# Optimization experiments

Hardware: AMD Instinct MI355X
Metric: run time of the kernel (lower is better)

## Reference

```python
import jax, jax.numpy as jnp
import numpy as np

H = 2048       # hidden_size
I = 5504       # intermediate_size
E = 8          # num_experts
TOPK = 2       # num_experts_per_tok


def setup_inputs() -> dict:
    key = jax.random.key(0)
    ks = jax.random.split(key, 5)
    s = 0.02
    x = jax.random.normal(ks[0], (2, 2048, H), dtype=jnp.float32)
    router_w = jax.random.normal(ks[1], (E, H), dtype=jnp.float32) * s   # Linear weight [out,in]
    Wg = jax.random.normal(ks[2], (E, I, H), dtype=jnp.float32) * s      # gate_proj per expert
    Wu = jax.random.normal(ks[3], (E, I, H), dtype=jnp.float32) * s      # up_proj per expert
    Wd = jax.random.normal(ks[4], (E, H, I), dtype=jnp.float32) * s      # down_proj per expert
    return {"x": x, "router_w": router_w, "Wg": Wg, "Wu": Wu, "Wd": Wd}


def reference(x, router_w, Wg, Wu, Wd):
    B, S, Hh = x.shape
    xf = x.reshape(-1, Hh)                                  # [T, H]
    logits = xf @ router_w.T                                # [T, E]
    top_vals, top_idx = jax.lax.top_k(logits, TOPK)         # [T, K]
    top_w = jax.nn.softmax(top_vals, axis=-1)               # softmax over selected logits only
    # combine weight per (token, expert): zero if expert not selected
    combine = jnp.sum(jax.nn.one_hot(top_idx, E, dtype=xf.dtype) * top_w[..., None], axis=1)  # [T, E]

    out = jnp.zeros_like(xf)
    for e in range(E):  # fixed small expert loop (unrolled under jit)
        h = jax.nn.silu(xf @ Wg[e].T) * (xf @ Wu[e].T)      # [T, I]
        y = h @ Wd[e].T                                     # [T, H]
        out = out + combine[:, e:e + 1] * y
    return out.reshape(B, S, Hh)
```

## Files before the change

kernel.cpp:

```cpp
#include <hip/hip_runtime.h>
#include <cstdint>
#include <cstddef>

#define HDIM 2048
#define IDIM 5504
#define NEXP 8
#define NTOK 4096
#define NROWS (2 * NTOK)

#define NCT1 86
#define NRT1 16
#define NWG1 (NCT1 * NRT1 * NEXP)
#define NCT2 16
#define NRT2 16
#define NWG2 (NCT2 * NRT2 * NEXP)

typedef _Float16 half8 __attribute__((ext_vector_type(8)));
typedef _Float16 half4v __attribute__((ext_vector_type(4)));
typedef float floatx4 __attribute__((ext_vector_type(4)));

#define GLOAD16(g, l)                                                         \
  __builtin_amdgcn_global_load_lds(                                           \
      (const __attribute__((address_space(1))) void*)(g),                     \
      (__attribute__((address_space(3))) void*)(l), 16, 0, 0)

#define XH_OFF   0
#define HB_OFF   (XH_OFF + (size_t)NTOK * HDIM * 2)
#define BTOK_OFF (HB_OFF + (size_t)NROWS * IDIM * 2)
#define BW_OFF   (BTOK_OFF + 32768)
#define TOKP_OFF (BW_OFF + 32768)
#define TOKW_OFF (TOKP_OFF + 16384)
#define T2R_OFF  (TOKW_OFF + 32768)
#define META_OFF (T2R_OFF + 32768)
#define Y2_OFF   (META_OFF + 128)
#define WS_NEED_Y2 (Y2_OFF + (size_t)NROWS * HDIM * 2)
#define WG16_OFF (WS_NEED_Y2)
#define WU16_OFF (WG16_OFF + (size_t)NEXP * IDIM * HDIM * 2)
#define WD16_OFF (WU16_OFF + (size_t)NEXP * IDIM * HDIM * 2)
#define WS_NEED_W16 (WD16_OFF + (size_t)NEXP * HDIM * IDIM * 2)


__global__ void cvt_x_kernel(const float4* __restrict__ x, half4v* __restrict__ xh, int n4) {
  int i = blockIdx.x * blockDim.x + threadIdx.x;
  int st = gridDim.x * blockDim.x;
  for (; i < n4; i += st) {
    float4 v = x[i];
    half4v o = { (_Float16)v.x, (_Float16)v.y, (_Float16)v.z, (_Float16)v.w };
    xh[i] = o;
  }
}

__global__ void cvt_w_kernel(const float4* __restrict__ w, half8* __restrict__ o, int n8) {
  int i = blockIdx.x * blockDim.x + threadIdx.x;
  int st = gridDim.x * blockDim.x;
  for (; i < n8; i += st) {
    float4 a = w[2 * i], b = w[2 * i + 1];
    o[i] = half8{ (_Float16)a.x, (_Float16)a.y, (_Float16)a.z, (_Float16)a.w,
                  (_Float16)b.x, (_Float16)b.y, (_Float16)b.z, (_Float16)b.w };
  }
}

__global__ void router_kernel(const float* __restrict__ x, const float* __restrict__ rw,
                              int* __restrict__ tokp, float2* __restrict__ tokw,
                              int* __restrict__ cnt) {
  int t = blockIdx.x * 4 + (threadIdx.x >> 6);
  int lane = threadIdx.x & 63;
  const float4* xr = (const float4*)(x + (size_t)t * HDIM);
  float acc[NEXP];
#pragma unroll
  for (int e = 0; e < NEXP; ++e) acc[e] = 0.f;
#pragma unroll
  for (int it = 0; it < HDIM / 256; ++it) {
    float4 xv = xr[lane + 64 * it];
#pragma unroll
    for (int e = 0; e < NEXP; ++e) {
      float4 wv = ((const float4*)(rw + (size_t)e * HDIM))[lane + 64 * it];
      acc[e] += xv.x * wv.x + xv.y * wv.y + xv.z * wv.z + xv.w * wv.w;
    }
  }
#pragma unroll
  for (int off = 32; off > 0; off >>= 1) {
#pragma unroll
    for (int e = 0; e < NEXP; ++e) acc[e] += __shfl_xor(acc[e], off);
  }
  if (lane == 0) {
    int e0 = 0; float v0 = acc[0];
#pragma unroll
    for (int e = 1; e < NEXP; ++e) {
      if (acc[e] > v0) { v0 = acc[e]; e0 = e; }
    }
    int e1 = -1; float v1 = -3.0e38f;
#pragma unroll
    for (int e = 0; e < NEXP; ++e) {
      if (e == e0) continue;
      if (acc[e] > v1) { v1 = acc[e]; e1 = e; }
    }
    float w0 = 1.f / (1.f + __expf(v1 - v0));
    tokp[t] = e0 | (e1 << 8);
    tokw[t] = make_float2(w0, 1.f - w0);
    atomicAdd(&cnt[e0], 1);
    atomicAdd(&cnt[e1], 1);
  }
}

__global__ void scan_kernel(const int* __restrict__ cnt, int* __restrict__ offp) {
  if (threadIdx.x == 0) {
    int s = 0;
    for (int e = 0; e < NEXP; ++e) { offp[e] = s; s += cnt[e]; }
    offp[NEXP] = s;
  }
}

__global__ void scatter_kernel(const int* __restrict__ tokp, const float2* __restrict__ tokw,
                               const int* __restrict__ offp, int* __restrict__ cursor,
                               int* __restrict__ btok, float* __restrict__ bw,
                               int* __restrict__ t2r) {
  int t = blockIdx.x * blockDim.x + threadIdx.x;
  if (t >= NTOK) return;
  int p = tokp[t];
  float2 w = tokw[t];
  int e0 = p & 0xff, e1 = (p >> 8) & 0xff;
  int r0 = offp[e0] + atomicAdd(&cursor[e0], 1);
  btok[r0] = t; bw[r0] = w.x; t2r[2 * t] = r0;
  int r1 = offp[e1] + atomicAdd(&cursor[e1], 1);
  btok[r1] = t; bw[r1] = w.y; t2r[2 * t + 1] = r1;
}

__global__ void combine_kernel(const _Float16* __restrict__ y2, const int* __restrict__ t2r,
                               const float2* __restrict__ tokw, float* __restrict__ out) {
  int idx = blockIdx.x * 256 + threadIdx.x;
  int t = idx >> 9, c = (idx & 511) * 4;
  int r0 = t2r[2 * t], r1 = t2r[2 * t + 1];
  float2 w = tokw[t];
  half4v v0 = *(const half4v*)(y2 + (size_t)r0 * HDIM + c);
  half4v v1 = *(const half4v*)(y2 + (size_t)r1 * HDIM + c);
  float4 o;
  o.x = w.x * (float)v0[0] + w.y * (float)v1[0];
  o.y = w.x * (float)v0[1] + w.y * (float)v1[1];
  o.z = w.x * (float)v0[2] + w.y * (float)v1[2];
  o.w = w.x * (float)v0[3] + w.y * (float)v1[3];
  *(float4*)(out + (size_t)t * HDIM + c) = o;
}

__global__ __launch_bounds__(256, 4) void stage1_kernel(
    const _Float16* __restrict__ xh, const _Float16* __restrict__ Wg16,
    const int* __restrict__ offp, const int* __restrict__ btok, _Float16* __restrict__ hb) {
  int bid = blockIdx.x;
  int wg = (bid & 7) * (NWG1 / 8) + (bid >> 3);
  int rt = wg % NRT1;
  int ct = (wg / NRT1) % NCT1;
  int e  = wg / (NRT1 * NCT1);
  int base = offp[e];
  int ne = offp[e + 1] - base;
  if (rt * 128 >= ne) return;
  int valid = ne - rt * 128; if (valid > 128) valid = 128;
  int tid = threadIdx.x, lane = tid & 63, wave = tid >> 6;

  __shared__ __attribute__((aligned(16))) _Float16 As[2][128 * 32];
  __shared__ __attribute__((aligned(16))) _Float16 Bs[2][128 * 32];

  const char* abase = (const char*)xh;
  const char* bbase = (const char*)(Wg16 + (size_t)e * IDIM * HDIM);

  uint32_t aoffB[2], boffB[2];
#pragma unroll
  for (int i = 0; i < 2; ++i) {
    int L = wave * 128 + i * 64 + lane;
    int u = L >> 3, sc = (L & 7) ^ (u & 7);
    int r = 2 * u + (sc >> 2), q = sc & 3;
    int rr = (r < valid) ? r : (valid - 1);
    aoffB[i] = (uint32_t)(((uint32_t)btok[base + rt * 128 + rr] * HDIM + q * 8) * 2);
    size_t eloff = (r < 64) ? ((size_t)(ct * 64 + r) * HDIM)
                            : ((size_t)NEXP * IDIM * HDIM + (size_t)(ct * 64 + (r - 64)) * HDIM);
    boffB[i] = (uint32_t)((eloff + (size_t)q * 8) * 2);
  }
  int adst0 = __builtin_amdgcn_readfirstlane(wave * 2048);

  int wm = wave >> 1, wn = wave & 1;
  int lrow = lane & 15, kg = lane >> 4;

  int aoff[4], boff[4];
#pragma unroll
  for (int mi = 0; mi < 4; ++mi) {
    int r = wm * 64 + mi * 16 + lrow;
    int u = r >> 1, cc = (r & 1) * 4 + kg;
    aoff[mi] = u * 64 + ((cc ^ (u & 7)) * 8);
  }
#pragma unroll
  for (int f = 0; f < 4; ++f) {
    int rb = (f < 2) ? (wn * 32 + f * 16 + lrow) : (64 + wn * 32 + (f - 2) * 16 + lrow);
    int u = rb >> 1, cc = (rb & 1) * 4 + kg;
    boff[f] = u * 64 + ((cc ^ (u & 7)) * 8);
  }

  floatx4 acc[4][4] = {};

  auto stage = [&](int t, int buf) {
    uint32_t kb = (uint32_t)t * 64u;
#pragma unroll
    for (int i = 0; i < 2; ++i) {
      GLOAD16(abase + (aoffB[i] + kb), (char*)As[buf] + adst0 + i * 1024);
      GLOAD16(bbase + (boffB[i] + kb), (char*)Bs[buf] + adst0 + i * 1024);
    }
  };
  auto compute = [&](int buf) {
    half8 af[4], bf[4];
#pragma unroll
    for (int mi = 0; mi < 4; ++mi) af[mi] = *(const half8*)&As[buf][aoff[mi]];
#pragma unroll
    for (int f = 0; f < 4; ++f) bf[f] = *(const half8*)&Bs[buf][boff[f]];
#pragma unroll
    for (int mi = 0; mi < 4; ++mi)
#pragma unroll
      for (int f = 0; f < 4; ++f)
        acc[mi][f] = __builtin_amdgcn_mfma_f32_16x16x32_f16(af[mi], bf[f], acc[mi][f], 0, 0, 0);
  };

  int cur = 0;
  stage(0, 0);
  __syncthreads();
#pragma unroll 2
  for (int t = 0; t < HDIM / 32 - 1; ++t) {
    stage(t + 1, cur ^ 1);
    compute(cur);
    __syncthreads();
    cur ^= 1;
  }
  compute(cur);

  size_t hrow_base = (size_t)(base + rt * 128);
#pragma unroll
  for (int mi = 0; mi < 4; ++mi) {
#pragma unroll
    for (int j = 0; j < 4; ++j) {
      int r = wm * 64 + mi * 16 + kg * 4 + j;
      if (r < valid) {
#pragma unroll
        for (int f = 0; f < 2; ++f) {
          float g = acc[mi][f][j], u = acc[mi][f + 2][j];
          float hv = g / (1.f + __expf(-g)) * u;
          int c = ct * 64 + wn * 32 + f * 16 + lrow;
          hb[(hrow_base + r) * IDIM + c] = (_Float16)hv;
        }
      }
    }
  }
}

__global__ __launch_bounds__(256, 4) void stage2_kernel(
    const _Float16* __restrict__ hb, const _Float16* __restrict__ Wd16,
    const int* __restrict__ offp, _Float16* __restrict__ y2) {
  int bid = blockIdx.x;
  int wg = (bid & 7) * (NWG2 / 8) + (bid >> 3);
  int rt = wg % NRT2;
  int ct = (wg / NRT2) % NCT2;
  int e  = wg / (NRT2 * NCT2);
  int base = offp[e];
  int ne = offp[e + 1] - base;
  if (rt * 128 >= ne) return;
  int valid = ne - rt * 128; if (valid > 128) valid = 128;
  int tid = threadIdx.x, lane = tid & 63, wave = tid >> 6;

  __shared__ __attribute__((aligned(16))) _Float16 As[2][128 * 32];
  __shared__ __attribute__((aligned(16))) _Float16 Bs[2][128 * 32];

  const char* abase = (const char*)hb;
  const char* bbase = (const char*)(Wd16 + (size_t)e * HDIM * IDIM);

  uint32_t aoffB[2], boffB[2];
#pragma unroll
  for (int i = 0; i < 2; ++i) {
    int L = wave * 128 + i * 64 + lane;
    int u = L >> 3, sc = (L & 7) ^ (u & 7);
    int r = 2 * u + (sc >> 2), q = sc & 3;
    int rr = (r < valid) ? r : (valid - 1);
    aoffB[i] = (uint32_t)(((size_t)(base + rt * 128 + rr) * IDIM + (size_t)q * 8) * 2);
    boffB[i] = (uint32_t)(((size_t)(ct * 128 + r) * IDIM + (size_t)q * 8) * 2);
  }
  int adst0 = __builtin_amdgcn_readfirstlane(wave * 2048);

  int wm = wave >> 1, wn = wave & 1;
  int lrow = lane & 15, kg = lane >> 4;

  int aoff[4], boff[4];
#pragma unroll
  for (int mi = 0; mi < 4; ++mi) {
    int r = wm * 64 + mi * 16 + lrow;
    int u = r >> 1, cc = (r & 1) * 4 + kg;
    aoff[mi] = u * 64 + ((cc ^ (u & 7)) * 8);
  }
#pragma unroll
  for (int f = 0; f < 4; ++f) {
    int rb = wn * 64 + f * 16 + lrow;
    int u = rb >> 1, cc = (rb & 1) * 4 + kg;
    boff[f] = u * 64 + ((cc ^ (u & 7)) * 8);
  }

  floatx4 acc[4][4] = {};

  auto stage = [&](int t, int buf) {
    uint32_t kb = (uint32_t)t * 64u;
#pragma unroll
    for (int i = 0; i < 2; ++i) {
      GLOAD16(abase + (aoffB[i] + kb), (char*)As[buf] + adst0 + i * 1024);
      GLOAD16(bbase + (boffB[i] + kb), (char*)Bs[buf] + adst0 + i * 1024);
    }
  };
  auto compute = [&](int buf) {
    half8 af[4], bf[4];
#pragma unroll
    for (int mi = 0; mi < 4; ++mi) af[mi] = *(const half8*)&As[buf][aoff[mi]];
#pragma unroll
    for (int f = 0; f < 4; ++f) bf[f] = *(const half8*)&Bs[buf][boff[f]];
#pragma unroll
    for (int mi = 0; mi < 4; ++mi)
#pragma unroll
      for (int f = 0; f < 4; ++f)
        acc[mi][f] = __builtin_amdgcn_mfma_f32_16x16x32_f16(af[mi], bf[f], acc[mi][f], 0, 0, 0);
  };

  int cur = 0;
  stage(0, 0);
  __syncthreads();
#pragma unroll 2
  for (int t = 0; t < IDIM / 32 - 1; ++t) {
    stage(t + 1, cur ^ 1);
    compute(cur);
    __syncthreads();
    cur ^= 1;
  }
  compute(cur);

#pragma unroll
  for (int mi = 0; mi < 4; ++mi) {
#pragma unroll
    for (int j = 0; j < 4; ++j) {
      int r = wm * 64 + mi * 16 + kg * 4 + j;
      if (r < valid) {
        int grow = base + rt * 128 + r;
#pragma unroll
        for (int f = 0; f < 4; ++f) {
          int c = ct * 128 + wn * 64 + f * 16 + lrow;
          y2[(size_t)grow * HDIM + c] = (_Float16)acc[mi][f][j];
        }
      }
    }
  }
}

extern "C" void kernel_launch(void* const* d_in, const int* in_sizes, int n_in,
                              void* d_out, int out_size, void* d_ws, size_t ws_size,
                              hipStream_t stream) {
  const float* x  = (const float*)d_in[0];
  const float* rw = (const float*)d_in[1];
  const float* Wg = (const float*)d_in[2];
  const float* Wu = (const float*)d_in[3];
  const float* Wd = (const float*)d_in[4];
  float* out = (float*)d_out;

  char* ws = (char*)d_ws;
  _Float16* xh  = (_Float16*)(ws + XH_OFF);
  _Float16* hb  = (_Float16*)(ws + HB_OFF);
  int*      btok = (int*)(ws + BTOK_OFF);
  float*    bwv  = (float*)(ws + BW_OFF);
  int*      tokp = (int*)(ws + TOKP_OFF);
  float2*   tokw = (float2*)(ws + TOKW_OFF);
  int*      t2r  = (int*)(ws + T2R_OFF);
  int*      meta = (int*)(ws + META_OFF);
  _Float16* y2   = (_Float16*)(ws + Y2_OFF);
  _Float16* wg16 = (_Float16*)(ws + WG16_OFF);
  _Float16* wu16 = (_Float16*)(ws + WU16_OFF);
  _Float16* wd16 = (_Float16*)(ws + WD16_OFF);
  int* cnt = meta;
  int* offp = meta + 8;
  int* cursor = meta + 20;

  hipMemsetAsync(meta, 0, 128, stream);

  cvt_x_kernel<<<2048, 256, 0, stream>>>((const float4*)x, (half4v*)xh, NTOK * HDIM / 4);
  router_kernel<<<NTOK / 4, 256, 0, stream>>>(x, rw, tokp, tokw, cnt);
  scan_kernel<<<1, 64, 0, stream>>>(cnt, offp);
  scatter_kernel<<<NTOK / 256, 256, 0, stream>>>(tokp, tokw, offp, cursor, btok, bwv, t2r);

  int n8 = NEXP * IDIM * HDIM / 8;
  cvt_w_kernel<<<2048, 256, 0, stream>>>((const float4*)Wg, (half8*)wg16, n8);
  cvt_w_kernel<<<2048, 256, 0, stream>>>((const float4*)Wu, (half8*)wu16, n8);
  cvt_w_kernel<<<2048, 256, 0, stream>>>((const float4*)Wd, (half8*)wd16, n8);

  stage1_kernel<<<NWG1, 256, 0, stream>>>(xh, wg16, offp, btok, hb);
  stage2_kernel<<<NWG2, 256, 0, stream>>>(hb, wd16, offp, y2);
  combine_kernel<<<NTOK * HDIM / 4 / 256, 256, 0, stream>>>(y2, t2r, tokw, out);
}
```

Baseline: 1.297 ms.

## Rewrite expert GEMMs as 256x256 tiles with 8-wave ping-pong pipeline

Both grouped GEMM stages go from 128x128 tiles with 4 waves and a simple double buffer to 256x256 tiles (split into four 128x128 quadrants) with 8 waves and K=64 per step. The main loop now uses manual s_barrier and vmcnt waits, staged half-tile global-to-LDS loads into four slots, and raised MFMA priority, so loads overlap with compute. The aim is more operand reuse per byte loaded and fewer synchronisation stalls. The cost is 128KB of LDS per block, heavy register pressure, and a fragile hand-tuned barrier and wait schedule. Partially filled row tiles at expert boundaries also waste more compute.

```diff
diff --git a/kernel.cpp b/kernel.cpp
--- a/kernel.cpp
+++ b/kernel.cpp
@@ -8,12 +8,14 @@
 #define NTOK 4096
 #define NROWS (2 * NTOK)
 
-#define NCT1 86
-#define NRT1 16
-#define NWG1 (NCT1 * NRT1 * NEXP)
-#define NCT2 16
-#define NRT2 16
-#define NWG2 (NCT2 * NRT2 * NEXP)
+#define S1_NCT 43
+#define S1_NRT 8
+#define S1_NWG (S1_NCT * S1_NRT * NEXP)
+#define S1_NK  (HDIM / 64)
+#define S2_NCT 8
+#define S2_NRT 8
+#define S2_NWG (S2_NCT * S2_NRT * NEXP)
+#define S2_NK  (IDIM / 64)
 
 typedef _Float16 half8 __attribute__((ext_vector_type(8)));
 typedef _Float16 half4v __attribute__((ext_vector_type(4)));
@@ -23,6 +25,9 @@
   __builtin_amdgcn_global_load_lds(                                           \
       (const __attribute__((address_space(1))) void*)(g),                     \
       (__attribute__((address_space(3))) void*)(l), 16, 0, 0)
+
+#define SBAR()  asm volatile("s_barrier" ::: "memory")
+#define VMCNT(n) asm volatile("s_waitcnt vmcnt(" #n ")" ::: "memory")
 
 #define XH_OFF   0
 #define HB_OFF   (XH_OFF + (size_t)NTOK * HDIM * 2)
@@ -37,7 +42,6 @@
 #define WG16_OFF (WS_NEED_Y2)
 #define WU16_OFF (WG16_OFF + (size_t)NEXP * IDIM * HDIM * 2)
 #define WD16_OFF (WU16_OFF + (size_t)NEXP * IDIM * HDIM * 2)
-#define WS_NEED_W16 (WD16_OFF + (size_t)NEXP * HDIM * IDIM * 2)
 
 
 __global__ void cvt_x_kernel(const float4* __restrict__ x, half4v* __restrict__ xh, int n4) {
@@ -142,206 +146,321 @@
   *(float4*)(out + (size_t)t * HDIM + c) = o;
 }
 
-__global__ __launch_bounds__(256, 4) void stage1_kernel(
+#define MFMA_Q(Q, BF)                                                          \
+  {                                                                            \
+    __builtin_amdgcn_s_setprio(1);                                             \
+    _Pragma("unroll") for (int mi = 0; mi < 4; ++mi)                           \
+      _Pragma("unroll") for (int ni = 0; ni < 2; ++ni)                         \
+        _Pragma("unroll") for (int kk = 0; kk < 2; ++kk)                       \
+          acc[Q][mi][ni] = __builtin_amdgcn_mfma_f32_16x16x32_f16(             \
+              af[mi][kk], BF[ni][kk], acc[Q][mi][ni], 0, 0, 0);                \
+    __builtin_amdgcn_s_setprio(0);                                             \
+  }
+
+__global__ __launch_bounds__(512, 2) void stage1_kernel(
     const _Float16* __restrict__ xh, const _Float16* __restrict__ Wg16,
     const int* __restrict__ offp, const int* __restrict__ btok, _Float16* __restrict__ hb) {
   int bid = blockIdx.x;
-  int wg = (bid & 7) * (NWG1 / 8) + (bid >> 3);
-  int rt = wg % NRT1;
-  int ct = (wg / NRT1) % NCT1;
-  int e  = wg / (NRT1 * NCT1);
+  int wg = (bid & 7) * (S1_NWG / 8) + (bid >> 3);
+  int rt = wg % S1_NRT;
+  int ct = (wg / S1_NRT) % S1_NCT;
+  int e  = wg / (S1_NRT * S1_NCT);
   int base = offp[e];
   int ne = offp[e + 1] - base;
-  if (rt * 128 >= ne) return;
-  int valid = ne - rt * 128; if (valid > 128) valid = 128;
+  if (rt * 256 >= ne) return;
+  int valid = ne - rt * 256; if (valid > 256) valid = 256;
   int tid = threadIdx.x, lane = tid & 63, wave = tid >> 6;
-
-  __shared__ __attribute__((aligned(16))) _Float16 As[2][128 * 32];
-  __shared__ __attribute__((aligned(16))) _Float16 Bs[2][128 * 32];
+  int qr = wave >> 2, qc = wave & 3;
+  int lrow = lane & 15, kg = lane >> 4;
+
+  __shared__ __attribute__((aligned(16))) _Float16 Ah[4][128 * 64];
+  __shared__ __attribute__((aligned(16))) _Float16 Bh[4][128 * 64];
 
   const char* abase = (const char*)xh;
   const char* bbase = (const char*)(Wg16 + (size_t)e * IDIM * HDIM);
 
-  uint32_t aoffB[2], boffB[2];
-#pragma unroll
-  for (int i = 0; i < 2; ++i) {
-    int L = wave * 128 + i * 64 + lane;
-    int u = L >> 3, sc = (L & 7) ^ (u & 7);
-    int r = 2 * u + (sc >> 2), q = sc & 3;
-    int rr = (r < valid) ? r : (valid - 1);
-    aoffB[i] = (uint32_t)(((uint32_t)btok[base + rt * 128 + rr] * HDIM + q * 8) * 2);
-    size_t eloff = (r < 64) ? ((size_t)(ct * 64 + r) * HDIM)
-                            : ((size_t)NEXP * IDIM * HDIM + (size_t)(ct * 64 + (r - 64)) * HDIM);
-    boffB[i] = (uint32_t)((eloff + (size_t)q * 8) * 2);
-  }
-  int adst0 = __builtin_amdgcn_readfirstlane(wave * 2048);
-
-  int wm = wave >> 1, wn = wave & 1;
-  int lrow = lane & 15, kg = lane >> 4;
-
-  int aoff[4], boff[4];
+  uint32_t aoffB[2][2], boffB[2][2];
+#pragma unroll
+  for (int half = 0; half < 2; ++half) {
+#pragma unroll
+    for (int i = 0; i < 2; ++i) {
+      int L = i * 512 + tid;
+      int r = L >> 3, c = (L & 7) ^ (r & 7);
+      int rl = half * 128 + r;
+      int rr = (rl < valid) ? rl : (valid - 1);
+      aoffB[half][i] = (uint32_t)(((uint32_t)btok[base + rt * 256 + rr] * HDIM + c * 8) * 2);
+      size_t off = ((size_t)ct * 128 + r) * HDIM + (size_t)c * 8;
+      if (half) off += (size_t)NEXP * IDIM * HDIM;
+      boffB[half][i] = (uint32_t)(off * 2);
+    }
+  }
+  int dst0 = wave * 1024;
+  int dst1 = 8192 + wave * 1024;
+
+  int aro[4][2], bro[2][2];
 #pragma unroll
   for (int mi = 0; mi < 4; ++mi) {
-    int r = wm * 64 + mi * 16 + lrow;
-    int u = r >> 1, cc = (r & 1) * 4 + kg;
-    aoff[mi] = u * 64 + ((cc ^ (u & 7)) * 8);
-  }
-#pragma unroll
-  for (int f = 0; f < 4; ++f) {
-    int rb = (f < 2) ? (wn * 32 + f * 16 + lrow) : (64 + wn * 32 + (f - 2) * 16 + lrow);
-    int u = rb >> 1, cc = (rb & 1) * 4 + kg;
-    boff[f] = u * 64 + ((cc ^ (u & 7)) * 8);
-  }
-
-  floatx4 acc[4][4] = {};
-
-  auto stage = [&](int t, int buf) {
-    uint32_t kb = (uint32_t)t * 64u;
-#pragma unroll
-    for (int i = 0; i < 2; ++i) {
-      GLOAD16(abase + (aoffB[i] + kb), (char*)As[buf] + adst0 + i * 1024);
-      GLOAD16(bbase + (boffB[i] + kb), (char*)Bs[buf] + adst0 + i * 1024);
-    }
-  };
-  auto compute = [&](int buf) {
-    half8 af[4], bf[4];
-#pragma unroll
-    for (int mi = 0; mi < 4; ++mi) af[mi] = *(const half8*)&As[buf][aoff[mi]];
-#pragma unroll
-    for (int f = 0; f < 4; ++f) bf[f] = *(const half8*)&Bs[buf][boff[f]];
+    int r = qr * 64 + mi * 16 + lrow;
+#pragma unroll
+    for (int kk = 0; kk < 2; ++kk)
+      aro[mi][kk] = (r * 8 + ((kk * 4 + kg) ^ (r & 7))) * 8;
+  }
+#pragma unroll
+  for (int ni = 0; ni < 2; ++ni) {
+    int r = qc * 32 + ni * 16 + lrow;
+#pragma unroll
+    for (int kk = 0; kk < 2; ++kk)
+      bro[ni][kk] = (r * 8 + ((kk * 4 + kg) ^ (r & 7))) * 8;
+  }
+
+  floatx4 acc[4][4][2] = {};
+  half8 af[4][2], b0f[2][2], b1f[2][2];
+
+  auto STA = [&](int t, int half, _Float16* slot) {
+    uint32_t kb = (uint32_t)((t < S1_NK) ? t : (S1_NK - 1)) * 128u;
+    GLOAD16(abase + (aoffB[half][0] + kb), (char*)slot + dst0);
+    GLOAD16(abase + (aoffB[half][1] + kb), (char*)slot + dst1);
+  };
+  auto STB = [&](int t, int half, _Float16* slot) {
+    uint32_t kb = (uint32_t)((t < S1_NK) ? t : (S1_NK - 1)) * 128u;
+    GLOAD16(bbase + (boffB[half][0] + kb), (char*)slot + dst0);
+    GLOAD16(bbase + (boffB[half][1] + kb), (char*)slot + dst1);
+  };
+  auto LDA = [&](const _Float16* slot) {
 #pragma unroll
     for (int mi = 0; mi < 4; ++mi)
 #pragma unroll
-      for (int f = 0; f < 4; ++f)
-        acc[mi][f] = __builtin_amdgcn_mfma_f32_16x16x32_f16(af[mi], bf[f], acc[mi][f], 0, 0, 0);
-  };
-
-  int cur = 0;
-  stage(0, 0);
-  __syncthreads();
-#pragma unroll 2
-  for (int t = 0; t < HDIM / 32 - 1; ++t) {
-    stage(t + 1, cur ^ 1);
-    compute(cur);
-    __syncthreads();
-    cur ^= 1;
-  }
-  compute(cur);
-
-  size_t hrow_base = (size_t)(base + rt * 128);
-#pragma unroll
-  for (int mi = 0; mi < 4; ++mi) {
-#pragma unroll
-    for (int j = 0; j < 4; ++j) {
-      int r = wm * 64 + mi * 16 + kg * 4 + j;
-      if (r < valid) {
-#pragma unroll
-        for (int f = 0; f < 2; ++f) {
-          float g = acc[mi][f][j], u = acc[mi][f + 2][j];
-          float hv = g / (1.f + __expf(-g)) * u;
-          int c = ct * 64 + wn * 32 + f * 16 + lrow;
-          hb[(hrow_base + r) * IDIM + c] = (_Float16)hv;
+      for (int kk = 0; kk < 2; ++kk) af[mi][kk] = *(const half8*)&slot[aro[mi][kk]];
+  };
+  auto LDB0 = [&](const _Float16* slot) {
+#pragma unroll
+    for (int ni = 0; ni < 2; ++ni)
+#pragma unroll
+      for (int kk = 0; kk < 2; ++kk) b0f[ni][kk] = *(const half8*)&slot[bro[ni][kk]];
+  };
+  auto LDB1 = [&](const _Float16* slot) {
+#pragma unroll
+    for (int ni = 0; ni < 2; ++ni)
+#pragma unroll
+      for (int kk = 0; kk < 2; ++kk) b1f[ni][kk] = *(const half8*)&slot[bro[ni][kk]];
+  };
+
+  STB(0, 0, Bh[0]); STA(0, 0, Ah[0]); STA(0, 1, Ah[1]); STB(0, 1, Bh[1]);
+
+  for (int I = 0; I < S1_NK / 2; ++I) {
+    int t1 = 2 * I + 1, t2 = 2 * I + 2;
+    STB(t1, 0, Bh[2]);
+    VMCNT(2);
+    SBAR();
+    LDA(Ah[0]); LDB0(Bh[0]);
+    MFMA_Q(0, b0f);
+    SBAR();
+    STA(t1, 0, Ah[2]);
+    SBAR();
+    LDB1(Bh[1]);
+    MFMA_Q(1, b1f);
+    SBAR();
+    STA(t1, 1, Ah[3]); STB(t1, 1, Bh[3]);
+    SBAR();
+    LDA(Ah[1]);
+    MFMA_Q(2, b0f);
+    SBAR();
+    SBAR();
+    MFMA_Q(3, b1f);
+    SBAR();
+    STB(t2, 0, Bh[0]);
+    VMCNT(6);
+    SBAR();
+    LDA(Ah[2]); LDB0(Bh[2]);
+    MFMA_Q(0, b0f);
+    SBAR();
+    STA(t2, 0, Ah[0]);
+    VMCNT(4);
+    SBAR();
+    LDB1(Bh[3]);
+    MFMA_Q(1, b1f);
+    SBAR();
+    STA(t2, 1, Ah[1]); STB(t2, 1, Bh[1]);
+    SBAR();
+    LDA(Ah[3]);
+    MFMA_Q(2, b0f);
+    SBAR();
+    SBAR();
+    MFMA_Q(3, b1f);
+    SBAR();
+  }
+
+  size_t hrow_base = (size_t)(base + rt * 256);
+#pragma unroll
+  for (int qrow = 0; qrow < 2; ++qrow) {
+#pragma unroll
+    for (int mi = 0; mi < 4; ++mi) {
+#pragma unroll
+      for (int j = 0; j < 4; ++j) {
+        int r = qrow * 128 + qr * 64 + mi * 16 + kg * 4 + j;
+        if (r < valid) {
+#pragma unroll
+          for (int ni = 0; ni < 2; ++ni) {
+            float g = acc[qrow * 2][mi][ni][j];
+            float u = acc[qrow * 2 + 1][mi][ni][j];
+            float hv = g / (1.f + __expf(-g)) * u;
+            int cidx = ct * 128 + qc * 32 + ni * 16 + lrow;
+            hb[(hrow_base + r) * IDIM + cidx] = (_Float16)hv;
+          }
         }
       }
     }
   }
 }
 
-__global__ __launch_bounds__(256, 4) void stage2_kernel(
+__global__ __launch_bounds__(512, 2) void stage2_kernel(
     const _Float16* __restrict__ hb, const _Float16* __restrict__ Wd16,
     const int* __restrict__ offp, _Float16* __restrict__ y2) {
   int bid = blockIdx.x;
-  int wg = (bid & 7) * (NWG2 / 8) + (bid >> 3);
-  int rt = wg % NRT2;
-  int ct = (wg / NRT2) % NCT2;
-  int e  = wg / (NRT2 * NCT2);
+  int wg = (bid & 7) * (S2_NWG / 8) + (bid >> 3);
+  int rt = wg % S2_NRT;
+  int ct = (wg / S2_NRT) % S2_NCT;
+  int e  = wg / (S2_NRT * S2_NCT);
   int base = offp[e];
   int ne = offp[e + 1] - base;
-  if (rt * 128 >= ne) return;
-  int valid = ne - rt * 128; if (valid > 128) valid = 128;
+  if (rt * 256 >= ne) return;
+  int valid = ne - rt * 256; if (valid > 256) valid = 256;
   int tid = threadIdx.x, lane = tid & 63, wave = tid >> 6;
-
-  __shared__ __attribute__((aligned(16))) _Float16 As[2][128 * 32];
-  __shared__ __attribute__((aligned(16))) _Float16 Bs[2][128 * 32];
+  int qr = wave >> 2, qc = wave & 3;
+  int lrow = lane & 15, kg = lane >> 4;
+
+  __shared__ __attribute__((aligned(16))) _Float16 Ah[4][128 * 64];
+  __shared__ __attribute__((aligned(16))) _Float16 Bh[4][128 * 64];
 
   const char* abase = (const char*)hb;
   const char* bbase = (const char*)(Wd16 + (size_t)e * HDIM * IDIM);
 
-  uint32_t aoffB[2], boffB[2];
-#pragma unroll
-  for (int i = 0; i < 2; ++i) {
-    int L = wave * 128 + i * 64 + lane;
-    int u = L >> 3, sc = (L & 7) ^ (u & 7);
-    int r = 2 * u + (sc >> 2), q = sc & 3;
-    int rr = (r < valid) ? r : (valid - 1);
-    aoffB[i] = (uint32_t)(((size_t)(base + rt * 128 + rr) * IDIM + (size_t)q * 8) * 2);
-    boffB[i] = (uint32_t)(((size_t)(ct * 128 + r) * IDIM + (size_t)q * 8) * 2);
-  }
-  int adst0 = __builtin_amdgcn_readfirstlane(wave * 2048);
-
-  int wm = wave >> 1, wn = wave & 1;
-  int lrow = lane & 15, kg = lane >> 4;
-
-  int aoff[4], boff[4];
+  uint32_t aoffB[2][2], boffB[2][2];
+#pragma unroll
+  for (int half = 0; half < 2; ++half) {
+#pragma unroll
+    for (int i = 0; i < 2; ++i) {
+      int L = i * 512 + tid;
+      int r = L >> 3, c = (L & 7) ^ (r & 7);
+      int rl = half * 128 + r;
+      int rr = (rl < valid) ? rl : (valid - 1);
+      aoffB[half][i] = (uint32_t)(((size_t)(base + rt * 256 + rr) * IDIM + (size_t)c * 8) * 2);
+      boffB[half][i] = (uint32_t)((((size_t)ct * 256 + half * 128 + r) * IDIM + (size_t)c * 8) * 2);
+    }
+  }
+  int dst0 = wave * 1024;
+  int dst1 = 8192 + wave * 1024;
+
+  int aro[4][2], bro[2][2];
 #pragma unroll
   for (int mi = 0; mi < 4; ++mi) {
-    int r = wm * 64 + mi * 16 + lrow;
-    int u = r >> 1, cc = (r & 1) * 4 + kg;
-    aoff[mi] = u * 64 + ((cc ^ (u & 7)) * 8);
-  }
-#pragma unroll
-  for (int f = 0; f < 4; ++f) {
-    int rb = wn * 64 + f * 16 + lrow;
-    int u = rb >> 1, cc = (rb & 1) * 4 + kg;
-    boff[f] = u * 64 + ((cc ^ (u & 7)) * 8);
-  }
-
-  floatx4 acc[4][4] = {};
-
-  auto stage = [&](int t, int buf) {
-    uint32_t kb = (uint32_t)t * 64u;
-#pragma unroll
-    for (int i = 0; i < 2; ++i) {
-      GLOAD16(abase + (aoffB[i] + kb), (char*)As[buf] + adst0 + i * 1024);
-      GLOAD16(bbase + (boffB[i] + kb), (char*)Bs[buf] + adst0 + i * 1024);
-    }
-  };
-  auto compute = [&](int buf) {
-    half8 af[4], bf[4];
-#pragma unroll
-    for (int mi = 0; mi < 4; ++mi) af[mi] = *(const half8*)&As[buf][aoff[mi]];
-#pragma unroll
-    for (int f = 0; f < 4; ++f) bf[f] = *(const half8*)&Bs[buf][boff[f]];
+    int r = qr * 64 + mi * 16 + lrow;
+#pragma unroll
+    for (int kk = 0; kk < 2; ++kk)
+      aro[mi][kk] = (r * 8 + ((kk * 4 + kg) ^ (r & 7))) * 8;
+  }
+#pragma unroll
+  for (int ni = 0; ni < 2; ++ni) {
+    int r = qc * 32 + ni * 16 + lrow;
+#pragma unroll
+    for (int kk = 0; kk < 2; ++kk)
+      bro[ni][kk] = (r * 8 + ((kk * 4 + kg) ^ (r & 7))) * 8;
+  }
+
+  floatx4 acc[4][4][2] = {};
+  half8 af[4][2], b0f[2][2], b1f[2][2];
+
+  auto STA = [&](int t, int half, _Float16* slot) {
+    uint32_t kb = (uint32_t)((t < S2_NK) ? t : (S2_NK - 1)) * 128u;
+    GLOAD16(abase + (aoffB[half][0] + kb), (char*)slot + dst0);
+    GLOAD16(abase + (aoffB[half][1] + kb), (char*)slot + dst1);
+  };
+  auto STB = [&](int t, int half, _Float16* slot) {
+    uint32_t kb = (uint32_t)((t < S2_NK) ? t : (S2_NK - 1)) * 128u;
+    GLOAD16(bbase + (boffB[half][0] + kb), (char*)slot + dst0);
+    GLOAD16(bbase + (boffB[half][1] + kb), (char*)slot + dst1);
+  };
+  auto LDA = [&](const _Float16* slot) {
 #pragma unroll
     for (int mi = 0; mi < 4; ++mi)
 #pragma unroll
-      for (int f = 0; f < 4; ++f)
-        acc[mi][f] = __builtin_amdgcn_mfma_f32_16x16x32_f16(af[mi], bf[f], acc[mi][f], 0, 0, 0);
-  };
-
-  int cur = 0;
-  stage(0, 0);
-  __syncthreads();
-#pragma unroll 2
-  for (int t = 0; t < IDIM / 32 - 1; ++t) {
-    stage(t + 1, cur ^ 1);
-    compute(cur);
-    __syncthreads();
-    cur ^= 1;
-  }
-  compute(cur);
-
-#pragma unroll
-  for (int mi = 0; mi < 4; ++mi) {
-#pragma unroll
-    for (int j = 0; j < 4; ++j) {
-      int r = wm * 64 + mi * 16 + kg * 4 + j;
-      if (r < valid) {
-        int grow = base + rt * 128 + r;
-#pragma unroll
-        for (int f = 0; f < 4; ++f) {
-          int c = ct * 128 + wn * 64 + f * 16 + lrow;
-          y2[(size_t)grow * HDIM + c] = (_Float16)acc[mi][f][j];
+      for (int kk = 0; kk < 2; ++kk) af[mi][kk] = *(const half8*)&slot[aro[mi][kk]];
+  };
+  auto LDB0 = [&](const _Float16* slot) {
+#pragma unroll
+    for (int ni = 0; ni < 2; ++ni)
+#pragma unroll
+      for (int kk = 0; kk < 2; ++kk) b0f[ni][kk] = *(const half8*)&slot[bro[ni][kk]];
+  };
+  auto LDB1 = [&](const _Float16* slot) {
+#pragma unroll
+    for (int ni = 0; ni < 2; ++ni)
+#pragma unroll
+      for (int kk = 0; kk < 2; ++kk) b1f[ni][kk] = *(const half8*)&slot[bro[ni][kk]];
+  };
+
+  STB(0, 0, Bh[0]); STA(0, 0, Ah[0]); STA(0, 1, Ah[1]); STB(0, 1, Bh[1]);
+
+  for (int I = 0; I < S2_NK / 2; ++I) {
+    int t1 = 2 * I + 1, t2 = 2 * I + 2;
+    STB(t1, 0, Bh[2]);
+    VMCNT(2);
+    SBAR();
+    LDA(Ah[0]); LDB0(Bh[0]);
+    MFMA_Q(0, b0f);
+    SBAR();
+    STA(t1, 0, Ah[2]);
+    SBAR();
+    LDB1(Bh[1]);
+    MFMA_Q(1, b1f);
+    SBAR();
+    STA(t1, 1, Ah[3]); STB(t1, 1, Bh[3]);
+    SBAR();
+    LDA(Ah[1]);
+    MFMA_Q(2, b0f);
+    SBAR();
+    SBAR();
+    MFMA_Q(3, b1f);
+    SBAR();
+    STB(t2, 0, Bh[0]);
+    VMCNT(6);
+    SBAR();
+    LDA(Ah[2]); LDB0(Bh[2]);
+    MFMA_Q(0, b0f);
+    SBAR();
+    STA(t2, 0, Ah[0]);
+    VMCNT(4);
+    SBAR();
+    LDB1(Bh[3]);
+    MFMA_Q(1, b1f);
+    SBAR();
+    STA(t2, 1, Ah[1]); STB(t2, 1, Bh[1]);
+    SBAR();
+    LDA(Ah[3]);
+    MFMA_Q(2, b0f);
+    SBAR();
+    SBAR();
+    MFMA_Q(3, b1f);
+    SBAR();
+  }
+
+#pragma unroll
+  for (int qrow = 0; qrow < 2; ++qrow) {
+#pragma unroll
+    for (int mi = 0; mi < 4; ++mi) {
+#pragma unroll
+      for (int j = 0; j < 4; ++j) {
+        int r = qrow * 128 + qr * 64 + mi * 16 + kg * 4 + j;
+        if (r < valid) {
+          size_t grow = (size_t)(base + rt * 256 + r);
+#pragma unroll
+          for (int qcol = 0; qcol < 2; ++qcol) {
+#pragma unroll
+            for (int ni = 0; ni < 2; ++ni) {
+              int cidx = ct * 256 + qcol * 128 + qc * 32 + ni * 16 + lrow;
+              y2[grow * HDIM + cidx] = (_Float16)acc[qrow * 2 + qcol][mi][ni][j];
+            }
+          }
         }
       }
     }
@@ -387,7 +506,7 @@
   cvt_w_kernel<<<2048, 256, 0, stream>>>((const float4*)Wu, (half8*)wu16, n8);
   cvt_w_kernel<<<2048, 256, 0, stream>>>((const float4*)Wd, (half8*)wd16, n8);
 
-  stage1_kernel<<<NWG1, 256, 0, stream>>>(xh, wg16, offp, btok, hb);
-  stage2_kernel<<<NWG2, 256, 0, stream>>>(hb, wd16, offp, y2);
+  stage1_kernel<<<S1_NWG, 512, 0, stream>>>(xh, wg16, offp, btok, hb);
+  stage2_kernel<<<S2_NWG, 512, 0, stream>>>(hb, wd16, offp, y2);
   combine_kernel<<<NTOK * HDIM / 4 / 256, 256, 0, stream>>>(y2, t2r, tokw, out);
 }
```

New measurement: 1.424 ms. +9.8%, slower.
